# Optimization experiments

Measured on AMD Instinct MI355X. Metric: run time of the kernel, lower is better.

The kernel has to match this reference:

```python
import jax, jax.numpy as jnp
import numpy as np

EPS = 1e-12  # tf.nn.l2_normalize epsilon

def _l2_normalize(x, axis):
    sq = jnp.sum(jnp.square(x), axis=axis, keepdims=True)
    return x * jax.lax.rsqrt(jnp.maximum(sq, EPS))

def setup_inputs() -> dict:
    key = jax.random.key(0)
    k1, k2 = jax.random.split(key)
    B, C, CLS = 8192, 512, 32000
    inputs = jax.random.normal(k1, (B, C), dtype=jnp.float32)
    # glorot_uniform for shape (C, CLS)
    limit = np.sqrt(6.0 / (C + CLS)).astype(np.float32)
    w = jax.random.uniform(k2, (C, CLS), dtype=jnp.float32, minval=-limit, maxval=limit)
    return {"inputs": inputs, "w": w}

def reference(inputs, w):
    # x: [B, C] l2-normalized over channel; w: [C, CLS] l2-normalized over channel.
    # The original broadcast-multiply-reduce over the channel axis == matmul.
    x = _l2_normalize(inputs, axis=-1)
    wn = _l2_normalize(w, axis=0)
    return jnp.einsum('bc,ck->bk', x, wn)  # [B, CLS] cosine similarities
```

## Files before the change

kernel.cpp:

```cpp
#include <hip/hip_runtime.h>
#include <hip/hip_bf16.h>
#include <stdint.h>

#define M_DIM 8192
#define K_DIM 512
#define N_DIM 32000

typedef short bf16x8 __attribute__((ext_vector_type(8)));
typedef float f32x4 __attribute__((ext_vector_type(4)));
typedef unsigned short u16;

__device__ __forceinline__ u16 f2bf(float f) {
  union { float f; uint32_t u; } v; v.f = f;
  uint32_t r = (v.u + 0x7fffu + ((v.u >> 16) & 1u)) >> 16;
  return (u16)r;
}

__global__ void k_zero(float* __restrict__ cn) {
  cn[blockIdx.x * 256 + threadIdx.x] = 0.f;
}

__global__ void k_xnorm(const float* __restrict__ x, u16* __restrict__ xn) {
  int row = (blockIdx.x * blockDim.x + threadIdx.x) >> 6;
  int lane = threadIdx.x & 63;
  const float4* rp = (const float4*)(x + (size_t)row * K_DIM);
  float4 a = rp[lane];
  float4 b = rp[lane + 64];
  float s = a.x*a.x + a.y*a.y + a.z*a.z + a.w*a.w
          + b.x*b.x + b.y*b.y + b.z*b.z + b.w*b.w;
#pragma unroll
  for (int off = 32; off > 0; off >>= 1) s += __shfl_xor(s, off, 64);
  float r = rsqrtf(fmaxf(s, 1e-12f));
  ushort4 o0 = make_ushort4(f2bf(a.x*r), f2bf(a.y*r), f2bf(a.z*r), f2bf(a.w*r));
  ushort4 o1 = make_ushort4(f2bf(b.x*r), f2bf(b.y*r), f2bf(b.z*r), f2bf(b.w*r));
  ushort4* dst = (ushort4*)(xn + (size_t)row * K_DIM);
  dst[lane] = o0;
  dst[lane + 64] = o1;
}

__global__ void k_wtrans(const float* __restrict__ w, float* __restrict__ cn,
                         u16* __restrict__ wT) {
  __shared__ u16 tile[64][68];
  int c0 = blockIdx.x * 64;
  int r0 = blockIdx.y * 64;
  int tc = threadIdx.x & 63;
  int tw = threadIdx.x >> 6;
  float s = 0.f;
#pragma unroll
  for (int i = 0; i < 16; ++i) {
    int r = i * 4 + tw;
    float v = w[(size_t)(r0 + r) * N_DIM + c0 + tc];
    s = fmaf(v, v, s);
    tile[tc][r] = f2bf(v);
  }
  atomicAdd(&cn[c0 + tc], s);
  __syncthreads();
  int cc = threadIdx.x >> 4;
  int rr = (threadIdx.x & 15) * 4;
#pragma unroll
  for (int i = 0; i < 4; ++i) {
    int c = cc + i * 16;
    ushort4 v = *(const ushort4*)&tile[c][rr];
    *(ushort4*)(wT + (size_t)(c0 + c) * K_DIM + r0 + rr) = v;
  }
}

__global__ __launch_bounds__(256, 2) void k_gemm(const u16* __restrict__ A,
                                                 const u16* __restrict__ Bt,
                                                 const float* __restrict__ cn,
                                                 float* __restrict__ C) {
  __shared__ u16 sm[2][16384];
  constexpr int BOFF = 8192;

  const int b = blockIdx.x;
  const int xcd = b & 7;
  const int blk = b >> 3;
  const int bm = xcd * 8 + (blk & 7);
  const int bn0 = blk >> 3;
  const int cnt = (bn0 < 2) ? 32 : 31;

  const int tid = threadIdx.x;
  const int lane = tid & 63;
  const int w = tid >> 6;
  const int wr = w >> 1;
  const int wc = w & 1;
  const int la = lane & 15;
  const int lk = lane >> 4;
  const int rx = la & 7;
  const int s0 = ((0 + lk) ^ rx) * 8;
  const int s1 = ((4 + lk) ^ rx) * 8;

  const int srow = tid >> 3;
  const int sgl = ((tid & 7) ^ (srow & 7)) * 8;
  const int ldst = srow * 64 + (tid & 7) * 8;
  const int arow0 = (wr * 64 + la) * 64;
  const int brow0 = (wc * 64 + la) * 64;

  const u16* ag = A + (size_t)(bm * 128 + srow) * K_DIM + sgl;
  int bn = bn0;
  const u16* bg = Bt + (size_t)(bn * 128 + srow) * K_DIM + sgl;
  constexpr size_t BSTEP = (size_t)8 * 128 * K_DIM;

  f32x4 acc[4][4] = {};

#define GLL(p, eoff)                                                              \
  __builtin_amdgcn_global_load_lds(                                              \
      (const __attribute__((address_space(1))) void*)(p),                        \
      (__attribute__((address_space(3))) void*)&sm[0][(eoff)], 16, 0, 0)

#pragma unroll
  for (int i = 0; i < 4; ++i) GLL(ag + (size_t)i * 32 * K_DIM, i * 2048 + ldst);
#pragma unroll
  for (int i = 0; i < 4; ++i) GLL(bg + (size_t)i * 32 * K_DIM, BOFF + i * 2048 + ldst);
  __syncthreads();

  for (int ti = 0; ti < cnt; ++ti) {
    const bool last_tile = (ti + 1 == cnt);

    for (int kt = 0; kt < 8; ++kt) {
      const int cur = kt & 1;
      const int nxt = cur ^ 1;
      const bool pf = (kt < 7) || !last_tile;
      const u16* agk = (kt < 7) ? (ag + (kt + 1) * 64) : ag;
      const u16* bgk = (kt < 7) ? (bg + (kt + 1) * 64) : (bg + BSTEP);

      if (pf) {
        const int nb = nxt * 16384;
#pragma unroll
        for (int i = 0; i < 4; ++i) GLL(agk + (size_t)i * 32 * K_DIM, nb + i * 2048 + ldst);
#pragma unroll
        for (int i = 0; i < 4; ++i) GLL(bgk + (size_t)i * 32 * K_DIM, nb + BOFF + i * 2048 + ldst);
      }

      bf16x8 af[4][2], bf[4][2];
#pragma unroll
      for (int m = 0; m < 4; ++m) {
        af[m][0] = *(const bf16x8*)&sm[cur][arow0 + m * 1024 + s0];
        af[m][1] = *(const bf16x8*)&sm[cur][arow0 + m * 1024 + s1];
      }
#pragma unroll
      for (int n = 0; n < 4; ++n) {
        bf[n][0] = *(const bf16x8*)&sm[cur][BOFF + brow0 + n * 1024 + s0];
        bf[n][1] = *(const bf16x8*)&sm[cur][BOFF + brow0 + n * 1024 + s1];
      }

#pragma unroll
      for (int m = 0; m < 4; ++m)
#pragma unroll
        for (int n = 0; n < 4; ++n) {
          acc[m][n] = __builtin_amdgcn_mfma_f32_16x16x32_bf16(af[m][0], bf[n][0], acc[m][n], 0, 0, 0);
          acc[m][n] = __builtin_amdgcn_mfma_f32_16x16x32_bf16(af[m][1], bf[n][1], acc[m][n], 0, 0, 0);
        }

      __syncthreads();
    }

    {
      const size_t crow0 = (size_t)bm * 128 + wr * 64 + lk * 4;
      const int ccol0 = bn * 128 + wc * 64 + la;
      float rs[4];
#pragma unroll
      for (int n = 0; n < 4; ++n)
        rs[n] = rsqrtf(fmaxf(cn[ccol0 + n * 16], 1e-12f));
#pragma unroll
      for (int m = 0; m < 4; ++m)
#pragma unroll
        for (int j = 0; j < 4; ++j) {
          float* cp = C + (crow0 + m * 16 + j) * N_DIM + ccol0;
#pragma unroll
          for (int n = 0; n < 4; ++n)
            __builtin_nontemporal_store(acc[m][n][j] * rs[n], cp + n * 16);
        }
#pragma unroll
      for (int m = 0; m < 4; ++m)
#pragma unroll
        for (int n = 0; n < 4; ++n)
          acc[m][n] = (f32x4){0.f, 0.f, 0.f, 0.f};
    }

    bn += 8;
    bg += BSTEP;
  }
#undef GLL
}

extern "C" void kernel_launch(void* const* d_in, const int* in_sizes, int n_in,
                              void* d_out, int out_size, void* d_ws, size_t ws_size,
                              hipStream_t stream) {
  const float* x = (const float*)d_in[0];
  const float* w = (const float*)d_in[1];
  float* out = (float*)d_out;

  char* ws = (char*)d_ws;
  float* cn = (float*)ws;
  u16* xn = (u16*)(ws + 131072);
  u16* wT = (u16*)(ws + 131072 + (size_t)M_DIM * K_DIM * 2);

  k_zero<<<N_DIM / 256, 256, 0, stream>>>(cn);
  k_xnorm<<<M_DIM / 4, 256, 0, stream>>>(x, xn);
  k_wtrans<<<dim3(N_DIM / 64, K_DIM / 64), 256, 0, stream>>>(w, cn, wT);
  k_gemm<<<512, 256, 0, stream>>>(xn, wT, cn, out);
}
```

Measured before the change: 355.8 us.

## Enlarge GEMM tile to 256x128 with K-step 32 and new LDS swizzle

Changes the persistent GEMM block tile from 128x128 to 256x128 (each wave computes 128x64), halves the K slice per stage to 32, and reworks the LDS layout and XOR swizzle to match. Each block now covers 4 M-tiles per XCD and walks 16-column strides, so A is reused across more N and B-tile loads per FLOP drop. It raises accumulator register pressure (128 accumulators per thread) under launch_bounds(256,2) and doubles the number of barriers per output tile, so spills or sync overhead may offset the gain.

```diff
diff --git a/kernel.cpp b/kernel.cpp
--- a/kernel.cpp
+++ b/kernel.cpp
@@ -69,15 +69,16 @@
                                                  const u16* __restrict__ Bt,
                                                  const float* __restrict__ cn,
                                                  float* __restrict__ C) {
-  __shared__ u16 sm[2][16384];
+  __shared__ u16 sm[2 * 12288];
   constexpr int BOFF = 8192;
+  constexpr int BUFE = 12288;
 
   const int b = blockIdx.x;
   const int xcd = b & 7;
   const int blk = b >> 3;
-  const int bm = xcd * 8 + (blk & 7);
-  const int bn0 = blk >> 3;
-  const int cnt = (bn0 < 2) ? 32 : 31;
+  const int bm = xcd * 4 + (blk & 3);
+  const int bn0 = blk >> 2;
+  const int cnt = (bn0 < 10) ? 16 : 15;
 
   const int tid = threadIdx.x;
   const int lane = tid & 63;
@@ -86,84 +87,76 @@
   const int wc = w & 1;
   const int la = lane & 15;
   const int lk = lane >> 4;
-  const int rx = la & 7;
-  const int s0 = ((0 + lk) ^ rx) * 8;
-  const int s1 = ((4 + lk) ^ rx) * 8;
+  const int sread = (lk ^ ((la >> 1) & 3)) * 8;
 
-  const int srow = tid >> 3;
-  const int sgl = ((tid & 7) ^ (srow & 7)) * 8;
-  const int ldst = srow * 64 + (tid & 7) * 8;
-  const int arow0 = (wr * 64 + la) * 64;
-  const int brow0 = (wc * 64 + la) * 64;
+  const int srow = tid >> 2;
+  const int sgl = ((tid & 3) ^ ((tid >> 3) & 3)) * 8;
+  const int ldst = tid * 8;
 
-  const u16* ag = A + (size_t)(bm * 128 + srow) * K_DIM + sgl;
+  const u16* ag = A + (size_t)(bm * 256 + srow) * K_DIM + sgl;
   int bn = bn0;
   const u16* bg = Bt + (size_t)(bn * 128 + srow) * K_DIM + sgl;
-  constexpr size_t BSTEP = (size_t)8 * 128 * K_DIM;
+  constexpr size_t BSTEP = (size_t)16 * 128 * K_DIM;
 
-  f32x4 acc[4][4] = {};
+  const int arow0 = (wr * 128 + la) * 32;
+  const int brow0 = (wc * 64 + la) * 32;
+
+  f32x4 acc[8][4] = {};
 
 #define GLL(p, eoff)                                                              \
   __builtin_amdgcn_global_load_lds(                                              \
       (const __attribute__((address_space(1))) void*)(p),                        \
-      (__attribute__((address_space(3))) void*)&sm[0][(eoff)], 16, 0, 0)
+      (__attribute__((address_space(3))) void*)&sm[(eoff)], 16, 0, 0)
 
 #pragma unroll
-  for (int i = 0; i < 4; ++i) GLL(ag + (size_t)i * 32 * K_DIM, i * 2048 + ldst);
+  for (int i = 0; i < 4; ++i) GLL(ag + (size_t)i * 64 * K_DIM, i * 2048 + ldst);
 #pragma unroll
-  for (int i = 0; i < 4; ++i) GLL(bg + (size_t)i * 32 * K_DIM, BOFF + i * 2048 + ldst);
+  for (int i = 0; i < 2; ++i) GLL(bg + (size_t)i * 64 * K_DIM, BOFF + i * 2048 + ldst);
   __syncthreads();
 
   for (int ti = 0; ti < cnt; ++ti) {
     const bool last_tile = (ti + 1 == cnt);
 
-    for (int kt = 0; kt < 8; ++kt) {
-      const int cur = kt & 1;
-      const int nxt = cur ^ 1;
-      const bool pf = (kt < 7) || !last_tile;
-      const u16* agk = (kt < 7) ? (ag + (kt + 1) * 64) : ag;
-      const u16* bgk = (kt < 7) ? (bg + (kt + 1) * 64) : (bg + BSTEP);
+    for (int kt = 0; kt < 16; ++kt) {
+      const int cur = (kt & 1) * BUFE;
+      const int nxt = cur ^ BUFE;
+      const bool pf = (kt < 15) || !last_tile;
+      const u16* agk = (kt < 15) ? (ag + (kt + 1) * 32) : ag;
+      const u16* bgk = (kt < 15) ? (bg + (kt + 1) * 32) : (bg + BSTEP);
 
       if (pf) {
-        const int nb = nxt * 16384;
 #pragma unroll
-        for (int i = 0; i < 4; ++i) GLL(agk + (size_t)i * 32 * K_DIM, nb + i * 2048 + ldst);
+        for (int i = 0; i < 4; ++i) GLL(agk + (size_t)i * 64 * K_DIM, nxt + i * 2048 + ldst);
 #pragma unroll
-        for (int i = 0; i < 4; ++i) GLL(bgk + (size_t)i * 32 * K_DIM, nb + BOFF + i * 2048 + ldst);
+        for (int i = 0; i < 2; ++i) GLL(bgk + (size_t)i * 64 * K_DIM, nxt + BOFF + i * 2048 + ldst);
       }
 
-      bf16x8 af[4][2], bf[4][2];
+      bf16x8 af[8], bf[4];
 #pragma unroll
-      for (int m = 0; m < 4; ++m) {
-        af[m][0] = *(const bf16x8*)&sm[cur][arow0 + m * 1024 + s0];
-        af[m][1] = *(const bf16x8*)&sm[cur][arow0 + m * 1024 + s1];
-      }
+      for (int m = 0; m < 8; ++m)
+        af[m] = *(const bf16x8*)&sm[cur + arow0 + m * 512 + sread];
 #pragma unroll
-      for (int n = 0; n < 4; ++n) {
-        bf[n][0] = *(const bf16x8*)&sm[cur][BOFF + brow0 + n * 1024 + s0];
-        bf[n][1] = *(const bf16x8*)&sm[cur][BOFF + brow0 + n * 1024 + s1];
-      }
+      for (int n = 0; n < 4; ++n)
+        bf[n] = *(const bf16x8*)&sm[cur + BOFF + brow0 + n * 512 + sread];
 
 #pragma unroll
-      for (int m = 0; m < 4; ++m)
+      for (int m = 0; m < 8; ++m)
 #pragma unroll
-        for (int n = 0; n < 4; ++n) {
-          acc[m][n] = __builtin_amdgcn_mfma_f32_16x16x32_bf16(af[m][0], bf[n][0], acc[m][n], 0, 0, 0);
-          acc[m][n] = __builtin_amdgcn_mfma_f32_16x16x32_bf16(af[m][1], bf[n][1], acc[m][n], 0, 0, 0);
-        }
+        for (int n = 0; n < 4; ++n)
+          acc[m][n] = __builtin_amdgcn_mfma_f32_16x16x32_bf16(af[m], bf[n], acc[m][n], 0, 0, 0);
 
       __syncthreads();
     }
 
     {
-      const size_t crow0 = (size_t)bm * 128 + wr * 64 + lk * 4;
+      const size_t crow0 = (size_t)bm * 256 + wr * 128 + lk * 4;
       const int ccol0 = bn * 128 + wc * 64 + la;
       float rs[4];
 #pragma unroll
       for (int n = 0; n < 4; ++n)
         rs[n] = rsqrtf(fmaxf(cn[ccol0 + n * 16], 1e-12f));
 #pragma unroll
-      for (int m = 0; m < 4; ++m)
+      for (int m = 0; m < 8; ++m)
 #pragma unroll
         for (int j = 0; j < 4; ++j) {
           float* cp = C + (crow0 + m * 16 + j) * N_DIM + ccol0;
@@ -172,13 +165,13 @@
             __builtin_nontemporal_store(acc[m][n][j] * rs[n], cp + n * 16);
         }
 #pragma unroll
-      for (int m = 0; m < 4; ++m)
+      for (int m = 0; m < 8; ++m)
 #pragma unroll
         for (int n = 0; n < 4; ++n)
           acc[m][n] = (f32x4){0.f, 0.f, 0.f, 0.f};
     }
 
-    bn += 8;
+    bn += 16;
     bg += BSTEP;
   }
 #undef GLL
```

New measurement: 393.0 us. +10.4%, slower.

## Load GEMM MFMA operands directly from global memory instead of LDS staging

Applied to the files above, without the earlier changes.

Removes the shared-memory double buffer, the global_load_lds prefetch and the per-k-step barriers from the GEMM kernel. Each wave now reads its A and B fragments straight from global memory into registers and relies on the L1/L2 caches for reuse across waves. The aim is to drop LDS traffic and synchronisation, at the cost of redundant global loads (A rows are shared by two waves, B rows by two waves), uncoalesced 16-byte strided accesses, and no explicit overlap of loads with MFMA work.

```diff
diff --git a/kernel.cpp b/kernel.cpp
--- a/kernel.cpp
+++ b/kernel.cpp
@@ -69,9 +69,6 @@
                                                  const u16* __restrict__ Bt,
                                                  const float* __restrict__ cn,
                                                  float* __restrict__ C) {
-  __shared__ u16 sm[2][16384];
-  constexpr int BOFF = 8192;
-
   const int b = blockIdx.x;
   const int xcd = b & 7;
   const int blk = b >> 3;
@@ -86,64 +83,35 @@
   const int wc = w & 1;
   const int la = lane & 15;
   const int lk = lane >> 4;
-  const int rx = la & 7;
-  const int s0 = ((0 + lk) ^ rx) * 8;
-  const int s1 = ((4 + lk) ^ rx) * 8;
 
-  const int srow = tid >> 3;
-  const int sgl = ((tid & 7) ^ (srow & 7)) * 8;
-  const int ldst = srow * 64 + (tid & 7) * 8;
-  const int arow0 = (wr * 64 + la) * 64;
-  const int brow0 = (wc * 64 + la) * 64;
+  const u16* aB[4];
+#pragma unroll
+  for (int m = 0; m < 4; ++m)
+    aB[m] = A + (size_t)(bm * 128 + wr * 64 + m * 16 + la) * K_DIM + lk * 8;
 
-  const u16* ag = A + (size_t)(bm * 128 + srow) * K_DIM + sgl;
   int bn = bn0;
-  const u16* bg = Bt + (size_t)(bn * 128 + srow) * K_DIM + sgl;
+  const size_t brow = (size_t)(wc * 64 + la) * K_DIM + lk * 8;
   constexpr size_t BSTEP = (size_t)8 * 128 * K_DIM;
+  const u16* bP = Bt + (size_t)(bn * 128) * K_DIM + brow;
+
+  const size_t crow0 = (size_t)bm * 128 + wr * 64 + lk * 4;
 
   f32x4 acc[4][4] = {};
 
-#define GLL(p, eoff)                                                              \
-  __builtin_amdgcn_global_load_lds(                                              \
-      (const __attribute__((address_space(1))) void*)(p),                        \
-      (__attribute__((address_space(3))) void*)&sm[0][(eoff)], 16, 0, 0)
-
+  for (int ti = 0; ti < cnt; ++ti) {
 #pragma unroll
-  for (int i = 0; i < 4; ++i) GLL(ag + (size_t)i * 32 * K_DIM, i * 2048 + ldst);
-#pragma unroll
-  for (int i = 0; i < 4; ++i) GLL(bg + (size_t)i * 32 * K_DIM, BOFF + i * 2048 + ldst);
-  __syncthreads();
-
-  for (int ti = 0; ti < cnt; ++ti) {
-    const bool last_tile = (ti + 1 == cnt);
-
     for (int kt = 0; kt < 8; ++kt) {
-      const int cur = kt & 1;
-      const int nxt = cur ^ 1;
-      const bool pf = (kt < 7) || !last_tile;
-      const u16* agk = (kt < 7) ? (ag + (kt + 1) * 64) : ag;
-      const u16* bgk = (kt < 7) ? (bg + (kt + 1) * 64) : (bg + BSTEP);
-
-      if (pf) {
-        const int nb = nxt * 16384;
-#pragma unroll
-        for (int i = 0; i < 4; ++i) GLL(agk + (size_t)i * 32 * K_DIM, nb + i * 2048 + ldst);
-#pragma unroll
-        for (int i = 0; i < 4; ++i) GLL(bgk + (size_t)i * 32 * K_DIM, nb + BOFF + i * 2048 + ldst);
-      }
-
       bf16x8 af[4][2], bf[4][2];
 #pragma unroll
       for (int m = 0; m < 4; ++m) {
-        af[m][0] = *(const bf16x8*)&sm[cur][arow0 + m * 1024 + s0];
-        af[m][1] = *(const bf16x8*)&sm[cur][arow0 + m * 1024 + s1];
+        af[m][0] = *(const bf16x8*)(aB[m] + kt * 64);
+        af[m][1] = *(const bf16x8*)(aB[m] + kt * 64 + 32);
       }
 #pragma unroll
       for (int n = 0; n < 4; ++n) {
-        bf[n][0] = *(const bf16x8*)&sm[cur][BOFF + brow0 + n * 1024 + s0];
-        bf[n][1] = *(const bf16x8*)&sm[cur][BOFF + brow0 + n * 1024 + s1];
+        bf[n][0] = *(const bf16x8*)(bP + (size_t)n * 16 * K_DIM + kt * 64);
+        bf[n][1] = *(const bf16x8*)(bP + (size_t)n * 16 * K_DIM + kt * 64 + 32);
       }
-
 #pragma unroll
       for (int m = 0; m < 4; ++m)
 #pragma unroll
@@ -151,12 +119,9 @@
           acc[m][n] = __builtin_amdgcn_mfma_f32_16x16x32_bf16(af[m][0], bf[n][0], acc[m][n], 0, 0, 0);
           acc[m][n] = __builtin_amdgcn_mfma_f32_16x16x32_bf16(af[m][1], bf[n][1], acc[m][n], 0, 0, 0);
         }
-
-      __syncthreads();
     }
 
     {
-      const size_t crow0 = (size_t)bm * 128 + wr * 64 + lk * 4;
       const int ccol0 = bn * 128 + wc * 64 + la;
       float rs[4];
 #pragma unroll
@@ -179,9 +144,8 @@
     }
 
     bn += 8;
-    bg += BSTEP;
+    bP += BSTEP;
   }
-#undef GLL
 }
 
 extern "C" void kernel_launch(void* const* d_in, const int* in_sizes, int n_in,
```

New measurement: 839.3 us. 136% more time.

## Replace LDS double buffering with single buffer and double GEMM occupancy

Applied to the files above, without the earlier changes.

Removes the double-buffered LDS staging in the GEMM in favor of a single 32KB buffer with load/sync/compute phases, and raises launch bounds to 4 blocks per CU with twice as many blocks, each covering half as many N tiles. Global-load latency is meant to be hidden by other resident blocks instead of by in-block prefetch. Fragment loads are restructured to hold fewer registers. It adds extra barriers per k-step and loses the in-block overlap of loads and MFMAs.

```diff
diff --git a/kernel.cpp b/kernel.cpp
--- a/kernel.cpp
+++ b/kernel.cpp
@@ -65,11 +65,11 @@
   }
 }
 
-__global__ __launch_bounds__(256, 2) void k_gemm(const u16* __restrict__ A,
+__global__ __launch_bounds__(256, 4) void k_gemm(const u16* __restrict__ A,
                                                  const u16* __restrict__ Bt,
                                                  const float* __restrict__ cn,
                                                  float* __restrict__ C) {
-  __shared__ u16 sm[2][16384];
+  __shared__ u16 sm[16384];
   constexpr int BOFF = 8192;
 
   const int b = blockIdx.x;
@@ -77,7 +77,7 @@
   const int blk = b >> 3;
   const int bm = xcd * 8 + (blk & 7);
   const int bn0 = blk >> 3;
-  const int cnt = (bn0 < 2) ? 32 : 31;
+  const int cnt = (bn0 < 10) ? 16 : 15;
 
   const int tid = threadIdx.x;
   const int lane = tid & 63;
@@ -99,60 +99,46 @@
   const u16* ag = A + (size_t)(bm * 128 + srow) * K_DIM + sgl;
   int bn = bn0;
   const u16* bg = Bt + (size_t)(bn * 128 + srow) * K_DIM + sgl;
-  constexpr size_t BSTEP = (size_t)8 * 128 * K_DIM;
+  constexpr size_t BSTEP = (size_t)16 * 128 * K_DIM;
 
   f32x4 acc[4][4] = {};
 
 #define GLL(p, eoff)                                                              \
   __builtin_amdgcn_global_load_lds(                                              \
       (const __attribute__((address_space(1))) void*)(p),                        \
-      (__attribute__((address_space(3))) void*)&sm[0][(eoff)], 16, 0, 0)
+      (__attribute__((address_space(3))) void*)&sm[(eoff)], 16, 0, 0)
+#define STAGE(pa, pb)                                                             \
+  { _Pragma("unroll")                                                             \
+    for (int i = 0; i < 4; ++i) GLL((pa) + (size_t)i * 32 * K_DIM, i * 2048 + ldst); \
+    _Pragma("unroll")                                                             \
+    for (int i = 0; i < 4; ++i) GLL((pb) + (size_t)i * 32 * K_DIM, BOFF + i * 2048 + ldst); }
 
-#pragma unroll
-  for (int i = 0; i < 4; ++i) GLL(ag + (size_t)i * 32 * K_DIM, i * 2048 + ldst);
-#pragma unroll
-  for (int i = 0; i < 4; ++i) GLL(bg + (size_t)i * 32 * K_DIM, BOFF + i * 2048 + ldst);
+  STAGE(ag, bg);
   __syncthreads();
 
   for (int ti = 0; ti < cnt; ++ti) {
-    const bool last_tile = (ti + 1 == cnt);
+    for (int kt = 0; kt < 8; ++kt) {
+#pragma unroll
+      for (int h = 0; h < 2; ++h) {
+        const int sh = h ? s1 : s0;
+        bf16x8 bfr[4];
+#pragma unroll
+        for (int n = 0; n < 4; ++n)
+          bfr[n] = *(const bf16x8*)&sm[BOFF + brow0 + n * 1024 + sh];
+#pragma unroll
+        for (int m = 0; m < 4; ++m) {
+          bf16x8 af = *(const bf16x8*)&sm[arow0 + m * 1024 + sh];
+#pragma unroll
+          for (int n = 0; n < 4; ++n)
+            acc[m][n] = __builtin_amdgcn_mfma_f32_16x16x32_bf16(af, bfr[n], acc[m][n], 0, 0, 0);
+        }
+      }
+      __syncthreads();
 
-    for (int kt = 0; kt < 8; ++kt) {
-      const int cur = kt & 1;
-      const int nxt = cur ^ 1;
-      const bool pf = (kt < 7) || !last_tile;
-      const u16* agk = (kt < 7) ? (ag + (kt + 1) * 64) : ag;
-      const u16* bgk = (kt < 7) ? (bg + (kt + 1) * 64) : (bg + BSTEP);
-
-      if (pf) {
-        const int nb = nxt * 16384;
-#pragma unroll
-        for (int i = 0; i < 4; ++i) GLL(agk + (size_t)i * 32 * K_DIM, nb + i * 2048 + ldst);
-#pragma unroll
-        for (int i = 0; i < 4; ++i) GLL(bgk + (size_t)i * 32 * K_DIM, nb + BOFF + i * 2048 + ldst);
+      if (kt < 7) {
+        STAGE(ag + (kt + 1) * 64, bg + (kt + 1) * 64);
+        __syncthreads();
       }
-
-      bf16x8 af[4][2], bf[4][2];
-#pragma unroll
-      for (int m = 0; m < 4; ++m) {
-        af[m][0] = *(const bf16x8*)&sm[cur][arow0 + m * 1024 + s0];
-        af[m][1] = *(const bf16x8*)&sm[cur][arow0 + m * 1024 + s1];
-      }
-#pragma unroll
-      for (int n = 0; n < 4; ++n) {
-        bf[n][0] = *(const bf16x8*)&sm[cur][BOFF + brow0 + n * 1024 + s0];
-        bf[n][1] = *(const bf16x8*)&sm[cur][BOFF + brow0 + n * 1024 + s1];
-      }
-
-#pragma unroll
-      for (int m = 0; m < 4; ++m)
-#pragma unroll
-        for (int n = 0; n < 4; ++n) {
-          acc[m][n] = __builtin_amdgcn_mfma_f32_16x16x32_bf16(af[m][0], bf[n][0], acc[m][n], 0, 0, 0);
-          acc[m][n] = __builtin_amdgcn_mfma_f32_16x16x32_bf16(af[m][1], bf[n][1], acc[m][n], 0, 0, 0);
-        }
-
-      __syncthreads();
     }
 
     {
@@ -178,10 +164,16 @@
           acc[m][n] = (f32x4){0.f, 0.f, 0.f, 0.f};
     }
 
-    bn += 8;
+    bn += 16;
     bg += BSTEP;
+
+    if (ti + 1 < cnt) {
+      STAGE(ag, bg);
+      __syncthreads();
+    }
   }
 #undef GLL
+#undef STAGE
 }
 
 extern "C" void kernel_launch(void* const* d_in, const int* in_sizes, int n_in,
@@ -199,5 +191,5 @@
   k_zero<<<N_DIM / 256, 256, 0, stream>>>(cn);
   k_xnorm<<<M_DIM / 4, 256, 0, stream>>>(x, xn);
   k_wtrans<<<dim3(N_DIM / 64, K_DIM / 64), 256, 0, stream>>>(w, cn, wT);
-  k_gemm<<<512, 256, 0, stream>>>(xn, wT, cn, out);
+  k_gemm<<<1024, 256, 0, stream>>>(xn, wT, cn, out);
 }
```

New measurement: 512.3 us. +44.0%, slower.
